# Performance work log

Hardware: AMD Instinct MI355X
Metric: run time of the kernel (lower is better)

Reference implementation:

```python
import jax, jax.numpy as jnp
import numpy as np

BATCH, C, BOX = 8, 1, 160
N, L = 20, 20


def setup_inputs() -> dict:
    key = jax.random.key(0)
    k1, k2, k3 = jax.random.split(key, 3)
    x = jax.random.normal(k1, (BATCH, C, BOX, BOX), dtype=jnp.float32)
    basis = jax.random.normal(k2, (N, L, 2, BOX, BOX), dtype=jnp.float32)
    angles = jax.random.uniform(k3, (BATCH,), dtype=jnp.float32) * (2.0 * np.pi)
    return {"x": x, "basis": basis, "angles": angles}


def reference(x, basis, angles):
    # euclid2basis: linear basis projection (GEMM in disguise)
    # coeffs: [b, c, N, L, 2]
    coeffs = jnp.einsum('bcij,nlrij->bcnlr', x, basis)

    # rotate: complex rotation of angular modes, angle scaled by harmonic index l
    l_mult = jnp.arange(L, dtype=x.dtype)                  # [L]
    ang = angles[:, None, None, None] * l_mult             # [b, 1, 1, L]
    ca, sa = jnp.cos(ang), jnp.sin(ang)
    a = coeffs[..., 0] * ca + coeffs[..., 1] * sa
    b = coeffs[..., 1] * ca - coeffs[..., 0] * sa
    rot = jnp.stack([a, b], axis=-1)                       # [b, c, N, L, 2]

    # basis2euclid: reconstruction (transpose GEMM)
    out = jnp.einsum('bcnlr,nlrij->bcij', rot, basis)      # [b, c, H, W]
    return out
```

## Files before the change

### kernel.cpp

```cpp
#include <hip/hip_runtime.h>
#include <math.h>

#define BATCH   8
#define LDIM    20
#define PIX     25600
#define NLPAIRS 400
#define NLR     800

#define PPB     256
#define NPX     (PIX / PPB)
#define RSPLIT  25

#define RPIX    64
#define RKS     8
#define RKLEN   (NLR / RKS)

__global__ __launch_bounds__(256) void proj_kernel(
    const float* __restrict__ x,
    const float* __restrict__ basis,
    float* __restrict__ part)
{
    const int tid   = threadIdx.x;
    const int lane  = tid & 63;
    const int wv    = tid >> 6;
    const int p     = blockIdx.x;
    const int rbase = blockIdx.y * 32 + wv * 8;
    const int px    = p * PPB + lane * 4;

    float4 xv[BATCH];
    #pragma unroll
    for (int b = 0; b < BATCH; ++b)
        xv[b] = *(const float4*)(x + (size_t)b * PIX + px);

    float4 bv[8];
    #pragma unroll
    for (int r = 0; r < 8; ++r)
        bv[r] = *(const float4*)(basis + (size_t)(rbase + r) * PIX + px);

    float v[64];
    #pragma unroll
    for (int r = 0; r < 8; ++r)
        #pragma unroll
        for (int b = 0; b < BATCH; ++b)
            v[r * 8 + b] = fmaf(bv[r].w, xv[b].w,
                           fmaf(bv[r].z, xv[b].z,
                           fmaf(bv[r].y, xv[b].y, bv[r].x * xv[b].x)));

    #pragma unroll
    for (int k = 0; k < 6; ++k) {
        const int m  = 1 << k;
        const int kb = (lane >> k) & 1;
        const int n  = 64 >> k;
        #pragma unroll
        for (int j = 0; j < 32; ++j) {
            if (j < n / 2) {
                float a    = v[2 * j];
                float c    = v[2 * j + 1];
                float send = kb ? a : c;
                float keep = kb ? c : a;
                v[j] = keep + __shfl_xor(send, m);
            }
        }
    }

    part[(size_t)p * (NLR * BATCH) + blockIdx.y * 256 + wv * 64 + lane] = v[0];
}

__global__ __launch_bounds__(256) void rotate_kernel(
    const float* __restrict__ part,
    const float* __restrict__ angles,
    float* __restrict__ rot)
{
    const int idx = blockIdx.x * 256 + threadIdx.x;
    const int nlr = idx >> 3;
    const int b   = idx & 7;

    float self = 0.0f;
    for (int p = 0; p < NPX; ++p)
        self += part[(size_t)p * (NLR * BATCH) + idx];

    float other = __shfl_xor(self, 8);

    const int l = (nlr >> 1) % LDIM;
    float ca, sa;
    __sincosf(angles[b] * (float)l, &sa, &ca);
    rot[idx] = (nlr & 1) == 0 ? fmaf(self, ca, other * sa)
                              : fmaf(self, ca, -other * sa);
}

__global__ __launch_bounds__(512) void recon_kernel(
    const float* __restrict__ basis,
    const float* __restrict__ rot,
    float* __restrict__ out)
{
    __shared__ float rl[NLR * BATCH];
    __shared__ float red[RKS - 1][BATCH][RPIX];

    const int tid = threadIdx.x;

    for (int idx = tid; idx < NLR * BATCH; idx += 512)
        rl[idx] = rot[idx];
    __syncthreads();

    const int lane = tid & 63;
    const int ks   = tid >> 6;
    const int pix  = blockIdx.x * RPIX + lane;

    float acc[BATCH];
    #pragma unroll
    for (int b = 0; b < BATCH; ++b) acc[b] = 0.0f;

    const float* __restrict__ bp = basis + (size_t)(ks * RKLEN) * PIX + pix;
    const float* __restrict__ rp = &rl[(ks * RKLEN) * BATCH];

    #pragma unroll 10
    for (int k = 0; k < RKLEN; ++k) {
        float bvv = bp[(size_t)k * PIX];
        float4 v0 = *(const float4*)&rp[k * BATCH];
        float4 v1 = *(const float4*)&rp[k * BATCH + 4];
        acc[0] = fmaf(bvv, v0.x, acc[0]);
        acc[1] = fmaf(bvv, v0.y, acc[1]);
        acc[2] = fmaf(bvv, v0.z, acc[2]);
        acc[3] = fmaf(bvv, v0.w, acc[3]);
        acc[4] = fmaf(bvv, v1.x, acc[4]);
        acc[5] = fmaf(bvv, v1.y, acc[5]);
        acc[6] = fmaf(bvv, v1.z, acc[6]);
        acc[7] = fmaf(bvv, v1.w, acc[7]);
    }

    if (ks > 0) {
        #pragma unroll
        for (int b = 0; b < BATCH; ++b)
            red[ks - 1][b][lane] = acc[b];
    }
    __syncthreads();

    if (ks == 0) {
        #pragma unroll
        for (int w = 0; w < RKS - 1; ++w)
            #pragma unroll
            for (int b = 0; b < BATCH; ++b)
                acc[b] += red[w][b][lane];
        #pragma unroll
        for (int b = 0; b < BATCH; ++b)
            out[(size_t)b * PIX + pix] = acc[b];
    }
}

extern "C" void kernel_launch(void* const* d_in, const int* in_sizes, int n_in,
                              void* d_out, int out_size, void* d_ws, size_t ws_size,
                              hipStream_t stream) {
    (void)in_sizes; (void)n_in; (void)ws_size; (void)out_size;

    const float* x      = (const float*)d_in[0];
    const float* basis  = (const float*)d_in[1];
    const float* angles = (const float*)d_in[2];
    float* out  = (float*)d_out;
    float* part = (float*)d_ws;
    float* rot  = part + (size_t)NPX * NLR * BATCH;

    proj_kernel<<<dim3(NPX, RSPLIT), dim3(256), 0, stream>>>(x, basis, part);
    rotate_kernel<<<dim3(NLR * BATCH / 256), dim3(256), 0, stream>>>(part, angles, rot);
    recon_kernel<<<dim3(PIX / RPIX), dim3(512), 0, stream>>>(basis, rot, out);
}
```

Baseline: 42.50 us.

## Replace partial-sum buffer with atomics and fuse rotation into reconstruction

```diff
diff --git a/kernel.cpp b/kernel.cpp
--- a/kernel.cpp
+++ b/kernel.cpp
@@ -18,7 +18,7 @@
 __global__ __launch_bounds__(256) void proj_kernel(
     const float* __restrict__ x,
     const float* __restrict__ basis,
-    float* __restrict__ part)
+    float* __restrict__ coeffs)
 {
     const int tid   = threadIdx.x;
     const int lane  = tid & 63;
@@ -63,34 +63,13 @@
         }
     }
 
-    part[(size_t)p * (NLR * BATCH) + blockIdx.y * 256 + wv * 64 + lane] = v[0];
-}
-
-__global__ __launch_bounds__(256) void rotate_kernel(
-    const float* __restrict__ part,
-    const float* __restrict__ angles,
-    float* __restrict__ rot)
-{
-    const int idx = blockIdx.x * 256 + threadIdx.x;
-    const int nlr = idx >> 3;
-    const int b   = idx & 7;
-
-    float self = 0.0f;
-    for (int p = 0; p < NPX; ++p)
-        self += part[(size_t)p * (NLR * BATCH) + idx];
-
-    float other = __shfl_xor(self, 8);
-
-    const int l = (nlr >> 1) % LDIM;
-    float ca, sa;
-    __sincosf(angles[b] * (float)l, &sa, &ca);
-    rot[idx] = (nlr & 1) == 0 ? fmaf(self, ca, other * sa)
-                              : fmaf(self, ca, -other * sa);
+    atomicAdd(&coeffs[(size_t)rbase * BATCH + lane], v[0]);
 }
 
 __global__ __launch_bounds__(512) void recon_kernel(
     const float* __restrict__ basis,
-    const float* __restrict__ rot,
+    const float* __restrict__ coeffs,
+    const float* __restrict__ angles,
     float* __restrict__ out)
 {
     __shared__ float rl[NLR * BATCH];
@@ -98,8 +77,17 @@
 
     const int tid = threadIdx.x;
 
-    for (int idx = tid; idx < NLR * BATCH; idx += 512)
-        rl[idx] = rot[idx];
+    for (int idx = tid; idx < NLR * BATCH; idx += 512) {
+        const int b   = idx & 7;
+        const int nlr = idx >> 3;
+        const int l   = (nlr >> 1) % LDIM;
+        float self  = coeffs[idx];
+        float other = coeffs[idx ^ 8];
+        float ca, sa;
+        __sincosf(angles[b] * (float)l, &sa, &ca);
+        rl[idx] = (nlr & 1) == 0 ? fmaf(self, ca, other * sa)
+                                 : fmaf(self, ca, -other * sa);
+    }
     __syncthreads();
 
     const int lane = tid & 63;
@@ -155,11 +143,11 @@
     const float* x      = (const float*)d_in[0];
     const float* basis  = (const float*)d_in[1];
     const float* angles = (const float*)d_in[2];
-    float* out  = (float*)d_out;
-    float* part = (float*)d_ws;
-    float* rot  = part + (size_t)NPX * NLR * BATCH;
+    float* out    = (float*)d_out;
+    float* coeffs = (float*)d_ws;
 
-    proj_kernel<<<dim3(NPX, RSPLIT), dim3(256), 0, stream>>>(x, basis, part);
-    rotate_kernel<<<dim3(NLR * BATCH / 256), dim3(256), 0, stream>>>(part, angles, rot);
-    recon_kernel<<<dim3(PIX / RPIX), dim3(512), 0, stream>>>(basis, rot, out);
+    hipMemsetAsync(d_ws, 0, (size_t)NLR * BATCH * sizeof(float), stream);
+
+    proj_kernel<<<dim3(NPX, RSPLIT), dim3(256), 0, stream>>>(x, basis, coeffs);
+    recon_kernel<<<dim3(PIX / RPIX), dim3(512), 0, stream>>>(basis, coeffs, angles, out);
 }
```

Measured after the change: 43.89 us. 1.03x slower.
